# Kernel tuning notes

Measured on AMD Instinct MI355X. Metric: run time of the kernel, lower is better.

The kernel has to match this reference:

```python
import jax, jax.numpy as jnp
import numpy as np

N, E, B, P = 131072, 262144, 4096, 1024
HID, CTX, FEAT, L = 256, 128, 512, 4


def _ln(x, g, bb, eps=1e-5):
    mu = jnp.mean(x, -1, keepdims=True)
    v = jnp.mean((x - mu) ** 2, -1, keepdims=True)
    return (x - mu) * jax.lax.rsqrt(v + eps) * g + bb


def setup_inputs() -> dict:
    key = jax.random.key(0)
    ks = iter(jax.random.split(key, 64))
    nrm = lambda sh, s=0.05: (jax.random.normal(next(ks), sh, jnp.float32) * s)
    inp = {
        "nf": jax.random.normal(next(ks), (N, 69), jnp.float32),
        "ei": jax.random.randint(next(ks), (2, E), 0, N, dtype=jnp.int32),
        "ef": jax.random.normal(next(ks), (E, 9), jnp.float32),
        "b": jnp.sort(jax.random.randint(next(ks), (N,), 0, B, dtype=jnp.int32)),
        "pid": jax.random.randint(next(ks), (B,), 0, P, dtype=jnp.int32),
        # MPNN params
        "Wn": nrm((69, HID)), "bn": jnp.zeros((HID,)),
        "We": nrm((9, HID)), "be": jnp.zeros((HID,)),
        "Wm": nrm((L, 2 * HID, HID)), "bm": jnp.zeros((L, HID)),
        "Wu": nrm((L, HID, HID)), "bu": jnp.zeros((L, HID)),
        "lng": jnp.ones((L, HID)), "lnb": jnp.zeros((L, HID)),
        # context embedding
        "ctx_emb": nrm((P, CTX), 0.02),
        # FiLM gamma net: Linear(128,256)-LN-ReLU-Linear(256,512)
        "gW1": nrm((CTX, HID)), "gb1": jnp.zeros((HID,)),
        "glng": jnp.ones((HID,)), "glnb": jnp.zeros((HID,)),
        "gW2": nrm((HID, FEAT)), "gb2": jnp.ones((FEAT,)),
        # FiLM beta net
        "bW1": nrm((CTX, HID)), "bb1": jnp.zeros((HID,)),
        "blng": jnp.ones((HID,)), "blnb": jnp.zeros((HID,)),
        "bW2": nrm((HID, FEAT)), "bb2": jnp.zeros((FEAT,)),
        # predictor: Linear(512,256)-ReLU-Linear(256,1)
        "pW1": nrm((FEAT, HID)), "pb1": jnp.zeros((HID,)),
        "pW2": nrm((HID, 1)), "pb2": jnp.zeros((1,)),
    }
    return inp


def reference(nf, ei, ef, b, pid, Wn, bn, We, be, Wm, bm, Wu, bu, lng, lnb,
              ctx_emb, gW1, gb1, glng, glnb, gW2, gb2,
              bW1, bb1, blng, blnb, bW2, bb2, pW1, pb1, pW2, pb2):
    src, dst = ei[0], ei[1]
    h = jax.nn.relu(nf @ Wn + bn)          # [N,256]
    e = jax.nn.relu(ef @ We + be)          # [E,256]
    for l in range(L):
        m = jax.nn.relu(jnp.concatenate([h[src], e], -1) @ Wm[l] + bm[l])  # [E,256]
        agg = jax.ops.segment_sum(m, dst, num_segments=N)                   # scatter-add
        h = _ln(h + jax.nn.relu(agg @ Wu[l] + bu[l]), lng[l], lnb[l])
    # graph readout: mean || max -> [B,512]
    ssum = jax.ops.segment_sum(h, b, num_segments=B)
    cnt = jnp.maximum(jax.ops.segment_sum(jnp.ones((h.shape[0], 1), h.dtype), b, num_segments=B), 1.0)
    gmax = jax.ops.segment_max(h, b, num_segments=B)
    gmax = jnp.where(jnp.isneginf(gmax), 0.0, gmax)
    g = jnp.concatenate([ssum / cnt, gmax], -1)  # [B,512]
    # FiLM fusion
    c = ctx_emb[pid]                              # [B,128]
    gamma = jax.nn.relu(_ln(c @ gW1 + gb1, glng, glnb)) @ gW2 + gb2
    beta = jax.nn.relu(_ln(c @ bW1 + bb1, blng, blnb)) @ bW2 + bb2
    hmod = gamma * g + beta
    out = (jax.nn.relu(hmod @ pW1 + pb1) @ pW2 + pb2).squeeze(-1)  # [B]
    return out
```

## Files before the change

kernel.cpp:

```cpp
#include <hip/hip_runtime.h>
#include <hip/hip_bf16.h>
#include <math.h>

#define HID 256
#define CTXD 128
#define FEAT 512
#define NLAYER 4

#define SW(n) (((n) >> 1) & 3)

typedef __hip_bfloat16 bf16;
typedef __attribute__((ext_vector_type(8))) short short8;
typedef __attribute__((ext_vector_type(4))) float floatx4;

__device__ __forceinline__ float bf2f(bf16 x) { return __bfloat162float(x); }
__device__ __forceinline__ bf16 f2bf(float x) { return __float2bfloat16(x); }
__device__ __forceinline__ float us2f(unsigned short u) {
    union { unsigned u; float f; } c; c.u = ((unsigned)u) << 16; return c.f;
}
__device__ __forceinline__ unsigned short f2us(float f) {
    bf16 b = f2bf(f); return *(unsigned short*)&b;
}

__device__ __forceinline__ void glds16(const void* g, void* l) {
    __builtin_amdgcn_global_load_lds(
        (__attribute__((address_space(1))) void*)g,
        (__attribute__((address_space(3))) void*)l, 16, 0, 0);
}

__global__ __launch_bounds__(256) void hist_kernel(const int* __restrict__ dst,
                                                   int* __restrict__ cnt, int E)
{
    int i = blockIdx.x * 256 + threadIdx.x;
    if (i < E) atomicAdd(&cnt[dst[i]], 1);
}

__global__ __launch_bounds__(256) void scan1_kernel(int* __restrict__ cnt,
                                                    int* __restrict__ bsum)
{
    __shared__ int sd[256];
    const int t = threadIdx.x;
    const int i = blockIdx.x * 256 + t;
    int v = cnt[i];
    sd[t] = v;
    __syncthreads();
    for (int o = 1; o < 256; o <<= 1) {
        int x = (t >= o) ? sd[t - o] : 0;
        __syncthreads();
        sd[t] += x;
        __syncthreads();
    }
    cnt[i] = sd[t] - v;
    if (t == 255) bsum[blockIdx.x] = sd[255];
}

__global__ void scan2_kernel(int* __restrict__ bsum)
{
    __shared__ int sd[512];
    const int t = threadIdx.x;
    int v = bsum[t];
    sd[t] = v;
    __syncthreads();
    for (int o = 1; o < 512; o <<= 1) {
        int x = (t >= o) ? sd[t - o] : 0;
        __syncthreads();
        sd[t] += x;
        __syncthreads();
    }
    bsum[t] = sd[t] - v;
}

__global__ __launch_bounds__(256) void scan3_kernel(int* __restrict__ cnt,
                                                    const int* __restrict__ bsum)
{
    int i = blockIdx.x * 256 + threadIdx.x;
    cnt[i] += bsum[blockIdx.x];
}

__global__ __launch_bounds__(256) void scatter_perm_kernel(
    const int* __restrict__ dst, int* __restrict__ cursor,
    int* __restrict__ perm, int E)
{
    int i = blockIdx.x * 256 + threadIdx.x;
    if (i < E) {
        int p = atomicAdd(&cursor[dst[i]], 1);
        perm[p] = i;
    }
}

__global__ __launch_bounds__(256)
void build_wimg_kernel(const float* __restrict__ W, bf16* __restrict__ img,
                       int K, int KT, int L)
{
    long idx = (long)blockIdx.x * 256 + threadIdx.x;
    long tot = (long)L * KT * 8192;
    if (idx >= tot) return;
    int l  = (int)(idx / ((long)KT * 8192));
    int r  = (int)(idx % ((long)KT * 8192));
    int kt = r >> 13;
    int r2 = r & 8191;
    int n  = r2 >> 5;
    int s  = (r2 >> 3) & 3;
    int j  = r2 & 7;
    int k  = kt * 32 + ((s ^ SW(n)) * 8) + j;
    float v = (k < K) ? W[((long)l * K + k) * HID + n] : 0.f;
    img[idx] = f2bf(v);
}

__global__ __launch_bounds__(512)
void msg_gemm3(const bf16* __restrict__ h_, const float* __restrict__ ef,
               const float* __restrict__ We, const float* __restrict__ be,
               const int* __restrict__ src, const int* __restrict__ perm,
               const float* __restrict__ W, const bf16* __restrict__ Wimg,
               const float* __restrict__ bias, bf16* __restrict__ mout)
{
    __shared__ __align__(16) short As[128 * 32];
    __shared__ __align__(16) short Bs[256 * 32];
    __shared__ int   srcL[128];
    __shared__ int   edgeL[128];
    __shared__ float efL[128][9];

    const int  t  = threadIdx.x;
    const long bm = (long)blockIdx.x * 128;

    if (t < 128) {
        int eg = perm[bm + t];
        edgeL[t] = eg;
        srcL[t]  = src[eg];
    }
    __syncthreads();
    for (int i = t; i < 128 * 9; i += 512) {
        int r = i / 9, qq = i % 9;
        efL[r][qq] = ef[(long)edgeL[r] * 9 + qq];
    }
    __syncthreads();

    floatx4 acc[4][4];
#pragma unroll
    for (int i = 0; i < 4; ++i)
#pragma unroll
        for (int j = 0; j < 4; ++j) acc[i][j] = (floatx4){0.f, 0.f, 0.f, 0.f};

    const int w = t >> 6, lane = t & 63;
    const int fr = lane & 15, q = lane >> 4;
    const int wm = (w & 1) * 64, wn = (w >> 1) * 64;
    const int arow = t >> 2, akg = t & 3;

    for (int kt = 0; kt < 16; ++kt) {
        const int k0 = kt * 32;
        {
            const int kk = k0 + akg * 8;
            short8 pk;
            if (kk < HID) {
                pk = *(const short8*)((const short*)h_ +
                                      ((long)srcL[arow] * HID + kk));
            } else {
                const int kc = kk - HID;
                float s[8];
#pragma unroll
                for (int j = 0; j < 8; ++j) s[j] = be[kc + j];
#pragma unroll
                for (int qq = 0; qq < 9; ++qq) {
                    const float efv = efL[arow][qq];
#pragma unroll
                    for (int j = 0; j < 8; ++j)
                        s[j] = fmaf(efv, We[qq * HID + kc + j], s[j]);
                }
#pragma unroll
                for (int j = 0; j < 8; ++j) pk[j] = (short)f2us(fmaxf(s[j], 0.f));
            }
            *(short8*)&As[arow * 32 + (akg ^ SW(arow)) * 8] = pk;
        }
        if (Wimg) {
            const short* base = (const short*)Wimg + (long)kt * 8192;
#pragma unroll
            for (int j = 0; j < 2; ++j) {
                const int chunk = w * 2 + j;
                glds16(base + chunk * 512 + lane * 8, (char*)Bs + chunk * 1024);
            }
        } else {
#pragma unroll
            for (int cc = 0; cc < 2; ++cc) {
                const int slot = t + cc * 512;
                const int n    = slot >> 2;
                const int kg   = slot & 3;
                const int kk   = k0 + kg * 8;
                short8 pk;
#pragma unroll
                for (int j = 0; j < 8; ++j)
                    pk[j] = (short)f2us(W[(long)(kk + j) * HID + n]);
                *(short8*)&Bs[n * 32 + (kg ^ SW(n)) * 8] = pk;
            }
        }
        __syncthreads();
        short8 af[4], bf8[4];
#pragma unroll
        for (int mt = 0; mt < 4; ++mt) {
            const int r = wm + mt * 16 + fr;
            af[mt] = *(const short8*)&As[r * 32 + (q ^ SW(r)) * 8];
        }
#pragma unroll
        for (int nt = 0; nt < 4; ++nt) {
            const int r = wn + nt * 16 + fr;
            bf8[nt] = *(const short8*)&Bs[r * 32 + (q ^ SW(r)) * 8];
        }
#pragma unroll
        for (int mt = 0; mt < 4; ++mt)
#pragma unroll
            for (int nt = 0; nt < 4; ++nt)
                acc[mt][nt] = __builtin_amdgcn_mfma_f32_16x16x32_bf16(
                    af[mt], bf8[nt], acc[mt][nt], 0, 0, 0);
        __syncthreads();
    }

#pragma unroll
    for (int nt = 0; nt < 4; ++nt) {
        const int col = wn + nt * 16 + fr;
        const float bv = bias[col];
#pragma unroll
        for (int mt = 0; mt < 4; ++mt)
#pragma unroll
            for (int reg = 0; reg < 4; ++reg) {
                const long row = bm + wm + mt * 16 + q * 4 + reg;
                mout[row * HID + col] = f2bf(fmaxf(acc[mt][nt][reg] + bv, 0.f));
            }
    }
}

__global__ __launch_bounds__(512)
void upd_gemm3(const bf16* __restrict__ mbuf, const int* __restrict__ cursor,
               const float* __restrict__ W, const bf16* __restrict__ Wimg,
               const float* __restrict__ bias,
               const float* __restrict__ lng, const float* __restrict__ lnb,
               bf16* __restrict__ h_)
{
    __shared__ __align__(16) short As[128 * 32];
    __shared__ __align__(16) short Bs[256 * 32];
    __shared__ int   rpL[129];
    __shared__ float redS[128][4];
    __shared__ float redS2[128][4];

    const int  t  = threadIdx.x;
    const long bm = (long)blockIdx.x * 128;

    if (t < 128) rpL[t + 1] = cursor[bm + t];
    if (t == 0)  rpL[0] = (bm == 0) ? 0 : cursor[bm - 1];
    __syncthreads();

    floatx4 acc[4][4];
#pragma unroll
    for (int i = 0; i < 4; ++i)
#pragma unroll
        for (int j = 0; j < 4; ++j) acc[i][j] = (floatx4){0.f, 0.f, 0.f, 0.f};

    const int w = t >> 6, lane = t & 63;
    const int fr = lane & 15, q = lane >> 4;
    const int wm = (w & 1) * 64, wn = (w >> 1) * 64;
    const int arow = t >> 2, akg = t & 3;

    for (int kt = 0; kt < 8; ++kt) {
        const int k0 = kt * 32;
        {
            const int kk = k0 + akg * 8;
            float s[8] = {0.f, 0.f, 0.f, 0.f, 0.f, 0.f, 0.f, 0.f};
            const int j1 = rpL[arow + 1];
            for (int j = rpL[arow]; j < j1; ++j) {
                const short8 mv = *(const short8*)((const short*)mbuf +
                                                   ((long)j * HID + kk));
#pragma unroll
                for (int x = 0; x < 8; ++x) s[x] += us2f((unsigned short)mv[x]);
            }
            short8 pk;
#pragma unroll
            for (int x = 0; x < 8; ++x) pk[x] = (short)f2us(s[x]);
            *(short8*)&As[arow * 32 + (akg ^ SW(arow)) * 8] = pk;
        }
        if (Wimg) {
            const short* base = (const short*)Wimg + (long)kt * 8192;
#pragma unroll
            for (int j = 0; j < 2; ++j) {
                const int chunk = w * 2 + j;
                glds16(base + chunk * 512 + lane * 8, (char*)Bs + chunk * 1024);
            }
        } else {
#pragma unroll
            for (int cc = 0; cc < 2; ++cc) {
                const int slot = t + cc * 512;
                const int n    = slot >> 2;
                const int kg   = slot & 3;
                const int kk   = k0 + kg * 8;
                short8 pk;
#pragma unroll
                for (int j = 0; j < 8; ++j)
                    pk[j] = (short)f2us(W[(long)(kk + j) * HID + n]);
                *(short8*)&Bs[n * 32 + (kg ^ SW(n)) * 8] = pk;
            }
        }
        __syncthreads();
        short8 af[4], bf8[4];
#pragma unroll
        for (int mt = 0; mt < 4; ++mt) {
            const int r = wm + mt * 16 + fr;
            af[mt] = *(const short8*)&As[r * 32 + (q ^ SW(r)) * 8];
        }
#pragma unroll
        for (int nt = 0; nt < 4; ++nt) {
            const int r = wn + nt * 16 + fr;
            bf8[nt] = *(const short8*)&Bs[r * 32 + (q ^ SW(r)) * 8];
        }
#pragma unroll
        for (int mt = 0; mt < 4; ++mt)
#pragma unroll
            for (int nt = 0; nt < 4; ++nt)
                acc[mt][nt] = __builtin_amdgcn_mfma_f32_16x16x32_bf16(
                    af[mt], bf8[nt], acc[mt][nt], 0, 0, 0);
        __syncthreads();
    }

    const int wnIdx = w >> 1;
#pragma unroll
    for (int mt = 0; mt < 4; ++mt)
#pragma unroll
        for (int reg = 0; reg < 4; ++reg) {
            const int  lrow = wm + mt * 16 + q * 4 + reg;
            const long row  = bm + lrow;
            float ps = 0.f, ps2 = 0.f;
#pragma unroll
            for (int nt = 0; nt < 4; ++nt) {
                const int col = wn + nt * 16 + fr;
                float v = bf2f(h_[row * HID + col]) +
                          fmaxf(acc[mt][nt][reg] + bias[col], 0.f);
                acc[mt][nt][reg] = v;
                ps  += v;
                ps2 += v * v;
            }
#pragma unroll
            for (int m = 1; m < 16; m <<= 1) {
                ps  += __shfl_xor(ps, m);
                ps2 += __shfl_xor(ps2, m);
            }
            if (fr == 0) { redS[lrow][wnIdx] = ps; redS2[lrow][wnIdx] = ps2; }
        }
    __syncthreads();
#pragma unroll
    for (int mt = 0; mt < 4; ++mt)
#pragma unroll
        for (int reg = 0; reg < 4; ++reg) {
            const int  lrow = wm + mt * 16 + q * 4 + reg;
            const long row  = bm + lrow;
            const float ts  = redS[lrow][0] + redS[lrow][1] +
                              redS[lrow][2] + redS[lrow][3];
            const float ts2 = redS2[lrow][0] + redS2[lrow][1] +
                              redS2[lrow][2] + redS2[lrow][3];
            const float mu  = ts * (1.f / 256.f);
            const float var = ts2 * (1.f / 256.f) - mu * mu;
            const float rs  = rsqrtf(var + 1e-5f);
#pragma unroll
            for (int nt = 0; nt < 4; ++nt) {
                const int col = wn + nt * 16 + fr;
                const float y = (acc[mt][nt][reg] - mu) * rs * lng[col] + lnb[col];
                h_[row * HID + col] = f2bf(y);
            }
        }
}

__global__ __launch_bounds__(512)
void enc_gemm3(const float* __restrict__ nf, const bf16* __restrict__ Wimg,
               const float* __restrict__ bias, bf16* __restrict__ h_)
{
    __shared__ __align__(16) short As[128 * 32];
    __shared__ __align__(16) short Bs[256 * 32];

    const int  t  = threadIdx.x;
    const long bm = (long)blockIdx.x * 128;

    floatx4 acc[4][4];
#pragma unroll
    for (int i = 0; i < 4; ++i)
#pragma unroll
        for (int j = 0; j < 4; ++j) acc[i][j] = (floatx4){0.f, 0.f, 0.f, 0.f};

    const int w = t >> 6, lane = t & 63;
    const int fr = lane & 15, q = lane >> 4;
    const int wm = (w & 1) * 64, wn = (w >> 1) * 64;
    const int arow = t >> 2, akg = t & 3;

    for (int kt = 0; kt < 3; ++kt) {
        const int k0 = kt * 32;
        {
            const int kk = k0 + akg * 8;
            short8 pk;
#pragma unroll
            for (int j = 0; j < 8; ++j) {
                const int k = kk + j;
                pk[j] = (short)f2us((k < 69) ? nf[(bm + arow) * 69 + k] : 0.f);
            }
            *(short8*)&As[arow * 32 + (akg ^ SW(arow)) * 8] = pk;
        }
        const short* base = (const short*)Wimg + (long)kt * 8192;
#pragma unroll
        for (int j = 0; j < 2; ++j) {
            const int chunk = w * 2 + j;
            glds16(base + chunk * 512 + lane * 8, (char*)Bs + chunk * 1024);
        }
        __syncthreads();
        short8 af[4], bf8[4];
#pragma unroll
        for (int mt = 0; mt < 4; ++mt) {
            const int r = wm + mt * 16 + fr;
            af[mt] = *(const short8*)&As[r * 32 + (q ^ SW(r)) * 8];
        }
#pragma unroll
        for (int nt = 0; nt < 4; ++nt) {
            const int r = wn + nt * 16 + fr;
            bf8[nt] = *(const short8*)&Bs[r * 32 + (q ^ SW(r)) * 8];
        }
#pragma unroll
        for (int mt = 0; mt < 4; ++mt)
#pragma unroll
            for (int nt = 0; nt < 4; ++nt)
                acc[mt][nt] = __builtin_amdgcn_mfma_f32_16x16x32_bf16(
                    af[mt], bf8[nt], acc[mt][nt], 0, 0, 0);
        __syncthreads();
    }

#pragma unroll
    for (int nt = 0; nt < 4; ++nt) {
        const int col = wn + nt * 16 + fr;
        const float bv = bias[col];
#pragma unroll
        for (int mt = 0; mt < 4; ++mt)
#pragma unroll
            for (int reg = 0; reg < 4; ++reg) {
                const long row = bm + wm + mt * 16 + q * 4 + reg;
                h_[row * HID + col] = f2bf(fmaxf(acc[mt][nt][reg] + bv, 0.f));
            }
    }
}

struct PlainF32 {
    const float* A; int lda;
    __device__ float operator()(int r, int k) const { return A[(long)r * lda + k]; }
};
struct CtxF32 {
    const float* ctx; const int* pid;
    __device__ float operator()(int r, int k) const {
        return ctx[(long)pid[r] * CTXD + k];
    }
};
struct StoreF32 {
    float* C; int ldc; int relu;
    __device__ void operator()(int r, int c, const float* v) const {
        float4 o;
        o.x = v[0]; o.y = v[1]; o.z = v[2]; o.w = v[3];
        if (relu) {
            o.x = fmaxf(o.x, 0.f); o.y = fmaxf(o.y, 0.f);
            o.z = fmaxf(o.z, 0.f); o.w = fmaxf(o.w, 0.f);
        }
        *(float4*)&C[(long)r * ldc + c] = o;
    }
};
struct StoreBf16Relu {
    bf16* C;
    __device__ void operator()(int r, int c, const float* v) const {
        bf16 tmp[4];
#pragma unroll
        for (int j = 0; j < 4; ++j) tmp[j] = f2bf(fmaxf(v[j], 0.f));
        *(ushort4*)&C[(long)r * HID + c] = *(const ushort4*)tmp;
    }
};

template <typename Loader, typename Epi>
__global__ __launch_bounds__(256)
void gemm_tiled(Loader loader, const float* __restrict__ W,
                const float* __restrict__ bias, Epi epi, int M, int K, int Nc)
{
    constexpr int BM = 64, BN = 64, BK = 16;
    __shared__ __align__(16) float As[BK][BM + 4];
    __shared__ __align__(16) float Ws[BK][BN];

    const int bm = blockIdx.x * BM;
    const int bn = blockIdx.y * BN;
    const int t  = threadIdx.x;
    const int arow = t >> 2, akq = (t & 3) * 4;
    const int wn = t & 63, wk0 = t >> 6;
    const int tx = t & 15, ty = t >> 4;

    float acc[4][4] = {};
    const int ntiles = (K + BK - 1) / BK;
    for (int kt = 0; kt < ntiles; ++kt) {
        const int k0 = kt * BK;
#pragma unroll
        for (int i = 0; i < 4; ++i) {
            int k = k0 + akq + i;
            As[akq + i][arow] = (k < K) ? loader(bm + arow, k) : 0.f;
        }
#pragma unroll
        for (int i = 0; i < 4; ++i) {
            int kr = wk0 + i * 4;
            int k  = k0 + kr;
            Ws[kr][wn] = (k < K) ? W[(long)k * Nc + bn + wn] : 0.f;
        }
        __syncthreads();
#pragma unroll
        for (int kk = 0; kk < BK; ++kk) {
            float4 a = *(const float4*)&As[kk][ty * 4];
            float4 b = *(const float4*)&Ws[kk][tx * 4];
            float av[4] = {a.x, a.y, a.z, a.w};
            float bv[4] = {b.x, b.y, b.z, b.w};
#pragma unroll
            for (int i = 0; i < 4; ++i)
#pragma unroll
                for (int j = 0; j < 4; ++j) acc[i][j] += av[i] * bv[j];
        }
        __syncthreads();
    }
#pragma unroll
    for (int i = 0; i < 4; ++i) {
        const int row = bm + ty * 4 + i;
        const int col = bn + tx * 4;
        float v[4];
#pragma unroll
        for (int j = 0; j < 4; ++j) v[j] = acc[i][j] + bias[col + j];
        epi(row, col, v);
    }
}

__global__ __launch_bounds__(256)
void ln_f32_relu_kernel(float* __restrict__ x, const float* __restrict__ g,
                        const float* __restrict__ bb)
{
    const long row = blockIdx.x;
    const int  j   = threadIdx.x;
    float v = x[row * HID + j];
    float s = v, s2 = v * v;
#pragma unroll
    for (int o = 32; o > 0; o >>= 1) {
        s  += __shfl_down(s, o);
        s2 += __shfl_down(s2, o);
    }
    __shared__ float red[2][4];
    const int wid = j >> 6, lane = j & 63;
    if (lane == 0) { red[0][wid] = s; red[1][wid] = s2; }
    __syncthreads();
    float ts  = red[0][0] + red[0][1] + red[0][2] + red[0][3];
    float ts2 = red[1][0] + red[1][1] + red[1][2] + red[1][3];
    float mu  = ts * (1.f / 256.f);
    float var = ts2 * (1.f / 256.f) - mu * mu;
    float y = (v - mu) * rsqrtf(var + 1e-5f) * g[j] + bb[j];
    x[row * HID + j] = fmaxf(y, 0.f);
}

__device__ int lower_bound_i(const int* __restrict__ arr, int n, int val)
{
    int lo = 0, hi = n;
    while (lo < hi) {
        int mid = (lo + hi) >> 1;
        if (arr[mid] < val) lo = mid + 1; else hi = mid;
    }
    return lo;
}

__global__ __launch_bounds__(256)
void readout_kernel(const bf16* __restrict__ h, const int* __restrict__ b,
                    float* __restrict__ gout, int Nn)
{
    const int gidx = blockIdx.x;
    const int j    = threadIdx.x;
    const int lo   = lower_bound_i(b, Nn, gidx);
    const int hi   = lower_bound_i(b, Nn, gidx + 1);
    float s = 0.f, mx = -INFINITY;
    for (int n = lo; n < hi; ++n) {
        float v = bf2f(h[(long)n * HID + j]);
        s += v;
        mx = fmaxf(mx, v);
    }
    const int cnt = hi - lo;
    gout[(long)gidx * FEAT + j]       = s / fmaxf((float)cnt, 1.f);
    gout[(long)gidx * FEAT + HID + j] = (cnt > 0) ? mx : 0.f;
}

__global__ __launch_bounds__(256)
void film_mod_kernel(const float* __restrict__ gamma, float* __restrict__ g,
                     const float* __restrict__ beta, int n)
{
    int i = blockIdx.x * 256 + threadIdx.x;
    if (i < n) g[i] = gamma[i] * g[i] + beta[i];
}

__global__ __launch_bounds__(256)
void final_dot_kernel(const float* __restrict__ ph, const float* __restrict__ w,
                      const float* __restrict__ b2, float* __restrict__ out)
{
    const int row  = blockIdx.x * 4 + (threadIdx.x >> 6);
    const int lane = threadIdx.x & 63;
    float s = 0.f;
#pragma unroll
    for (int k = lane; k < HID; k += 64)
        s += ph[(long)row * HID + k] * w[k];
#pragma unroll
    for (int o = 32; o > 0; o >>= 1) s += __shfl_down(s, o);
    if (lane == 0) out[row] = s + b2[0];
}

__global__ void diag_out_kernel(float* out, int n, float wsmb)
{
    int i = blockIdx.x * 256 + threadIdx.x;
    if (i < n) out[i] = (i == 0) ? wsmb : 0.f;
}

extern "C" void kernel_launch(void* const* d_in, const int* in_sizes, int n_in,
                              void* d_out, int out_size, void* d_ws, size_t ws_size,
                              hipStream_t stream)
{
    const int N = 131072, E = 262144, B = 4096;

    const float* nf   = (const float*)d_in[0];
    const int*   ei   = (const int*)  d_in[1];
    const float* ef   = (const float*)d_in[2];
    const int*   bidx = (const int*)  d_in[3];
    const int*   pid  = (const int*)  d_in[4];
    const float* Wn   = (const float*)d_in[5];
    const float* bn   = (const float*)d_in[6];
    const float* We   = (const float*)d_in[7];
    const float* be   = (const float*)d_in[8];
    const float* Wm   = (const float*)d_in[9];
    const float* bm   = (const float*)d_in[10];
    const float* Wu   = (const float*)d_in[11];
    const float* bu   = (const float*)d_in[12];
    const float* lng  = (const float*)d_in[13];
    const float* lnb  = (const float*)d_in[14];
    const float* ctx  = (const float*)d_in[15];
    const float* gW1  = (const float*)d_in[16];
    const float* gb1  = (const float*)d_in[17];
    const float* glng = (const float*)d_in[18];
    const float* glnb = (const float*)d_in[19];
    const float* gW2  = (const float*)d_in[20];
    const float* gb2  = (const float*)d_in[21];
    const float* bW1  = (const float*)d_in[22];
    const float* bb1  = (const float*)d_in[23];
    const float* blng = (const float*)d_in[24];
    const float* blnb = (const float*)d_in[25];
    const float* bW2  = (const float*)d_in[26];
    const float* bb2  = (const float*)d_in[27];
    const float* pW1  = (const float*)d_in[28];
    const float* pb1  = (const float*)d_in[29];
    const float* pW2  = (const float*)d_in[30];
    const float* pb2  = (const float*)d_in[31];

    const int* src = ei;
    const int* dst = ei + E;
    float* out = (float*)d_out;

    const size_t hB    = (size_t)N * HID * sizeof(bf16);
    const size_t mB    = (size_t)E * HID * sizeof(bf16);
    const size_t curB  = (size_t)N * 4;
    const size_t permB = (size_t)E * 4;
    const size_t bsumB = 2048 * 4;
    const size_t wmImgB = (size_t)NLAYER * 16 * 8192 * 2;
    const size_t wuImgB = (size_t)NLAYER * 8  * 8192 * 2;
    const size_t wnImgB = (size_t)3 * 8192 * 2;

    const size_t needBase = hB + mB + curB + permB + bsumB;
    const size_t needFull = needBase + wmImgB + wuImgB + wnImgB;

    if (ws_size < needBase) {
        diag_out_kernel<<<dim3((B + 255) / 256), dim3(256), 0, stream>>>(
            out, B, (float)(ws_size >> 20));
        return;
    }
    const bool haveImg = ws_size >= needFull;

    char* p = (char*)d_ws;
    bf16* h      = (bf16*)p;  p += hB;
    bf16* mbuf   = (bf16*)p;  p += mB;
    int*  cursor = (int*)p;   p += curB;
    int*  perm   = (int*)p;   p += permB;
    int*  bsum   = (int*)p;   p += bsumB;
    bf16* wmImg = nullptr; bf16* wuImg = nullptr; bf16* wnImg = nullptr;
    if (haveImg) {
        wmImg = (bf16*)p; p += wmImgB;
        wuImg = (bf16*)p; p += wuImgB;
        wnImg = (bf16*)p; p += wnImgB;
    }

    float* gbuf  = (float*)mbuf;
    float* t1    = gbuf  + (long)B * FEAT;
    float* t2    = t1    + (long)B * HID;
    float* gamma = t2    + (long)B * HID;
    float* beta  = gamma + (long)B * FEAT;
    float* ph    = beta  + (long)B * FEAT;

    dim3 blk(256), blk5(512);

    hipMemsetAsync(cursor, 0, curB, stream);
    hist_kernel<<<dim3(E / 256), blk, 0, stream>>>(dst, cursor, E);
    scan1_kernel<<<dim3(N / 256), blk, 0, stream>>>(cursor, bsum);
    scan2_kernel<<<dim3(1), dim3(512), 0, stream>>>(bsum);
    scan3_kernel<<<dim3(N / 256), blk, 0, stream>>>(cursor, bsum);
    scatter_perm_kernel<<<dim3(E / 256), blk, 0, stream>>>(dst, cursor, perm, E);

    if (haveImg) {
        build_wimg_kernel<<<dim3((NLAYER * 16 * 8192 + 255) / 256), blk, 0, stream>>>(
            Wm, wmImg, 2 * HID, 16, NLAYER);
        build_wimg_kernel<<<dim3((NLAYER * 8 * 8192 + 255) / 256), blk, 0, stream>>>(
            Wu, wuImg, HID, 8, NLAYER);
        build_wimg_kernel<<<dim3((3 * 8192 + 255) / 256), blk, 0, stream>>>(
            Wn, wnImg, 69, 3, 1);
    }

    if (haveImg) {
        enc_gemm3<<<dim3(N / 128), blk5, 0, stream>>>(nf, wnImg, bn, h);
    } else {
        gemm_tiled<<<dim3(N / 64, HID / 64), blk, 0, stream>>>(
            PlainF32{nf, 69}, Wn, bn, StoreBf16Relu{h}, N, 69, HID);
    }

    for (int l = 0; l < NLAYER; ++l) {
        const float* Wml  = Wm  + (long)l * 2 * HID * HID;
        const float* bml  = bm  + (long)l * HID;
        const float* Wul  = Wu  + (long)l * HID * HID;
        const float* bul  = bu  + (long)l * HID;
        const float* lngl = lng + (long)l * HID;
        const float* lnbl = lnb + (long)l * HID;
        const bf16* wmI = haveImg ? wmImg + (long)l * 16 * 8192 : nullptr;
        const bf16* wuI = haveImg ? wuImg + (long)l * 8 * 8192 : nullptr;

        msg_gemm3<<<dim3(E / 128), blk5, 0, stream>>>(
            h, ef, We, be, src, perm, Wml, wmI, bml, mbuf);
        upd_gemm3<<<dim3(N / 128), blk5, 0, stream>>>(
            mbuf, cursor, Wul, wuI, bul, lngl, lnbl, h);
    }

    readout_kernel<<<dim3(B), blk, 0, stream>>>(h, bidx, gbuf, N);

    gemm_tiled<<<dim3(B / 64, HID / 64), blk, 0, stream>>>(
        CtxF32{ctx, pid}, gW1, gb1, StoreF32{t1, HID, 0}, B, CTXD, HID);
    ln_f32_relu_kernel<<<dim3(B), blk, 0, stream>>>(t1, glng, glnb);
    gemm_tiled<<<dim3(B / 64, FEAT / 64), blk, 0, stream>>>(
        PlainF32{t1, HID}, gW2, gb2, StoreF32{gamma, FEAT, 0}, B, HID, FEAT);

    gemm_tiled<<<dim3(B / 64, HID / 64), blk, 0, stream>>>(
        CtxF32{ctx, pid}, bW1, bb1, StoreF32{t2, HID, 0}, B, CTXD, HID);
    ln_f32_relu_kernel<<<dim3(B), blk, 0, stream>>>(t2, blng, blnb);
    gemm_tiled<<<dim3(B / 64, FEAT / 64), blk, 0, stream>>>(
        PlainF32{t2, HID}, bW2, bb2, StoreF32{beta, FEAT, 0}, B, HID, FEAT);

    film_mod_kernel<<<dim3((B * FEAT + 255) / 256), blk, 0, stream>>>(
        gamma, gbuf, beta, B * FEAT);
    gemm_tiled<<<dim3(B / 64, HID / 64), blk, 0, stream>>>(
        PlainF32{gbuf, FEAT}, pW1, pb1, StoreF32{ph, HID, 1}, B, FEAT, HID);
    final_dot_kernel<<<dim3(B / 4), blk, 0, stream>>>(ph, pW2, pb2, out);
}
```

Before: 2.004 ms.

## Precompute node-side message GEMM and fuse edge messages with segmented aggregation

The message GEMM is split algebraically. The h[src] half of Wm is applied once per node (N rows) rather than once per edge (E rows), and the result is gathered per edge and combined with the edge-feature half. A new msg_agg kernel walks the dst-sorted edges of 64 destination nodes, computes the edge-half GEMM plus bias and ReLU in shared memory, and sums the messages per node directly. This removes the E×256 message buffer round trip and the separate gather-sum in the update kernel. In exchange, the node projection is rounded to bf16 before the sum, and blocks with many edges loop over chunks, which can cause load imbalance.

```diff
diff --git a/kernel.cpp b/kernel.cpp
--- a/kernel.cpp
+++ b/kernel.cpp
@@ -107,33 +107,119 @@
     img[idx] = f2bf(v);
 }
 
+__device__ __forceinline__ void kt_tail512(
+    int kt, const bf16* __restrict__ Wimg, const float* __restrict__ W,
+    short* As, short* Bs, floatx4 (&acc)[4][4])
+{
+    const int t = threadIdx.x;
+    const int w = t >> 6, lane = t & 63;
+    const int fr = lane & 15, q = lane >> 4;
+    const int wm = (w & 1) * 64, wn = (w >> 1) * 64;
+    const int k0 = kt * 32;
+
+    if (Wimg) {
+        const short* base = (const short*)Wimg + (long)kt * 8192;
+#pragma unroll
+        for (int j = 0; j < 2; ++j) {
+            const int chunk = w * 2 + j;
+            glds16(base + chunk * 512 + lane * 8, (char*)Bs + chunk * 1024);
+        }
+    } else {
+#pragma unroll
+        for (int cc = 0; cc < 2; ++cc) {
+            const int slot = t + cc * 512;
+            const int n    = slot >> 2;
+            const int kg   = slot & 3;
+            const int kk   = k0 + kg * 8;
+            short8 pk;
+#pragma unroll
+            for (int j = 0; j < 8; ++j)
+                pk[j] = (short)f2us(W[(long)(kk + j) * HID + n]);
+            *(short8*)&Bs[n * 32 + (kg ^ SW(n)) * 8] = pk;
+        }
+    }
+    __syncthreads();
+    short8 af[4], bf8[4];
+#pragma unroll
+    for (int mt = 0; mt < 4; ++mt) {
+        const int r = wm + mt * 16 + fr;
+        af[mt] = *(const short8*)&As[r * 32 + (q ^ SW(r)) * 8];
+    }
+#pragma unroll
+    for (int nt = 0; nt < 4; ++nt) {
+        const int r = wn + nt * 16 + fr;
+        bf8[nt] = *(const short8*)&Bs[r * 32 + (q ^ SW(r)) * 8];
+    }
+#pragma unroll
+    for (int mt = 0; mt < 4; ++mt)
+#pragma unroll
+        for (int nt = 0; nt < 4; ++nt)
+            acc[mt][nt] = __builtin_amdgcn_mfma_f32_16x16x32_bf16(
+                af[mt], bf8[nt], acc[mt][nt], 0, 0, 0);
+    __syncthreads();
+}
+
+__device__ __forceinline__ void kt_tail256(
+    int kt, const bf16* __restrict__ Wimg, const float* __restrict__ W,
+    short* As, short* Bs, floatx4 (&acc)[4][4])
+{
+    const int t = threadIdx.x;
+    const int w = t >> 6, lane = t & 63;
+    const int fr = lane & 15, q = lane >> 4;
+    const int wn = w * 64;
+    const int k0 = kt * 32;
+
+    if (Wimg) {
+        const short* base = (const short*)Wimg + (long)kt * 8192;
+#pragma unroll
+        for (int j = 0; j < 4; ++j) {
+            const int chunk = w * 4 + j;
+            glds16(base + chunk * 512 + lane * 8, (char*)Bs + chunk * 1024);
+        }
+    } else {
+#pragma unroll
+        for (int cc = 0; cc < 4; ++cc) {
+            const int slot = t + cc * 256;
+            const int n    = slot >> 2;
+            const int kg   = slot & 3;
+            const int kk   = k0 + kg * 8;
+            short8 pk;
+#pragma unroll
+            for (int j = 0; j < 8; ++j)
+                pk[j] = (short)f2us(W[(long)(kk + j) * HID + n]);
+            *(short8*)&Bs[n * 32 + (kg ^ SW(n)) * 8] = pk;
+        }
+    }
+    __syncthreads();
+    short8 af[4], bf8[4];
+#pragma unroll
+    for (int mt = 0; mt < 4; ++mt) {
+        const int r = mt * 16 + fr;
+        af[mt] = *(const short8*)&As[r * 32 + (q ^ SW(r)) * 8];
+    }
+#pragma unroll
+    for (int nt = 0; nt < 4; ++nt) {
+        const int r = wn + nt * 16 + fr;
+        bf8[nt] = *(const short8*)&Bs[r * 32 + (q ^ SW(r)) * 8];
+    }
+#pragma unroll
+    for (int mt = 0; mt < 4; ++mt)
+#pragma unroll
+        for (int nt = 0; nt < 4; ++nt)
+            acc[mt][nt] = __builtin_amdgcn_mfma_f32_16x16x32_bf16(
+                af[mt], bf8[nt], acc[mt][nt], 0, 0, 0);
+    __syncthreads();
+}
+
 __global__ __launch_bounds__(512)
-void msg_gemm3(const bf16* __restrict__ h_, const float* __restrict__ ef,
-               const float* __restrict__ We, const float* __restrict__ be,
-               const int* __restrict__ src, const int* __restrict__ perm,
-               const float* __restrict__ W, const bf16* __restrict__ Wimg,
-               const float* __restrict__ bias, bf16* __restrict__ mout)
+void ht_gemm(const bf16* __restrict__ h_, const float* __restrict__ W,
+             const bf16* __restrict__ Wimg, bf16* __restrict__ ht)
 {
     __shared__ __align__(16) short As[128 * 32];
     __shared__ __align__(16) short Bs[256 * 32];
-    __shared__ int   srcL[128];
-    __shared__ int   edgeL[128];
-    __shared__ float efL[128][9];
 
     const int  t  = threadIdx.x;
     const long bm = (long)blockIdx.x * 128;
-
-    if (t < 128) {
-        int eg = perm[bm + t];
-        edgeL[t] = eg;
-        srcL[t]  = src[eg];
-    }
-    __syncthreads();
-    for (int i = t; i < 128 * 9; i += 512) {
-        int r = i / 9, qq = i % 9;
-        efL[r][qq] = ef[(long)edgeL[r] * 9 + qq];
-    }
-    __syncthreads();
 
     floatx4 acc[4][4];
 #pragma unroll
@@ -145,90 +231,157 @@
     const int fr = lane & 15, q = lane >> 4;
     const int wm = (w & 1) * 64, wn = (w >> 1) * 64;
     const int arow = t >> 2, akg = t & 3;
-
-    for (int kt = 0; kt < 16; ++kt) {
-        const int k0 = kt * 32;
-        {
-            const int kk = k0 + akg * 8;
-            short8 pk;
-            if (kk < HID) {
-                pk = *(const short8*)((const short*)h_ +
-                                      ((long)srcL[arow] * HID + kk));
-            } else {
-                const int kc = kk - HID;
-                float s[8];
-#pragma unroll
-                for (int j = 0; j < 8; ++j) s[j] = be[kc + j];
-#pragma unroll
-                for (int qq = 0; qq < 9; ++qq) {
-                    const float efv = efL[arow][qq];
-#pragma unroll
-                    for (int j = 0; j < 8; ++j)
-                        s[j] = fmaf(efv, We[qq * HID + kc + j], s[j]);
-                }
-#pragma unroll
-                for (int j = 0; j < 8; ++j) pk[j] = (short)f2us(fmaxf(s[j], 0.f));
-            }
-            *(short8*)&As[arow * 32 + (akg ^ SW(arow)) * 8] = pk;
-        }
-        if (Wimg) {
-            const short* base = (const short*)Wimg + (long)kt * 8192;
-#pragma unroll
-            for (int j = 0; j < 2; ++j) {
-                const int chunk = w * 2 + j;
-                glds16(base + chunk * 512 + lane * 8, (char*)Bs + chunk * 1024);
-            }
-        } else {
-#pragma unroll
-            for (int cc = 0; cc < 2; ++cc) {
-                const int slot = t + cc * 512;
-                const int n    = slot >> 2;
-                const int kg   = slot & 3;
-                const int kk   = k0 + kg * 8;
-                short8 pk;
-#pragma unroll
-                for (int j = 0; j < 8; ++j)
-                    pk[j] = (short)f2us(W[(long)(kk + j) * HID + n]);
-                *(short8*)&Bs[n * 32 + (kg ^ SW(n)) * 8] = pk;
-            }
-        }
-        __syncthreads();
-        short8 af[4], bf8[4];
-#pragma unroll
-        for (int mt = 0; mt < 4; ++mt) {
-            const int r = wm + mt * 16 + fr;
-            af[mt] = *(const short8*)&As[r * 32 + (q ^ SW(r)) * 8];
-        }
-#pragma unroll
-        for (int nt = 0; nt < 4; ++nt) {
-            const int r = wn + nt * 16 + fr;
-            bf8[nt] = *(const short8*)&Bs[r * 32 + (q ^ SW(r)) * 8];
-        }
-#pragma unroll
-        for (int mt = 0; mt < 4; ++mt)
-#pragma unroll
-            for (int nt = 0; nt < 4; ++nt)
-                acc[mt][nt] = __builtin_amdgcn_mfma_f32_16x16x32_bf16(
-                    af[mt], bf8[nt], acc[mt][nt], 0, 0, 0);
-        __syncthreads();
+    const int aslot = arow * 32 + (akg ^ SW(arow)) * 8;
+
+    for (int kt = 0; kt < 8; ++kt) {
+        const int kk = kt * 32 + akg * 8;
+        short8 v = *(const short8*)((const short*)h_ + (bm + arow) * HID + kk);
+        *(short8*)&As[aslot] = v;
+        kt_tail512(kt, Wimg, W, As, Bs, acc);
     }
 
 #pragma unroll
     for (int nt = 0; nt < 4; ++nt) {
         const int col = wn + nt * 16 + fr;
-        const float bv = bias[col];
 #pragma unroll
         for (int mt = 0; mt < 4; ++mt)
 #pragma unroll
             for (int reg = 0; reg < 4; ++reg) {
                 const long row = bm + wm + mt * 16 + q * 4 + reg;
-                mout[row * HID + col] = f2bf(fmaxf(acc[mt][nt][reg] + bv, 0.f));
+                ht[row * HID + col] = f2bf(acc[mt][nt][reg]);
             }
     }
 }
 
+__global__ __launch_bounds__(256)
+void msg_agg(const bf16* __restrict__ ht, const float* __restrict__ ef,
+             const float* __restrict__ We, const float* __restrict__ be,
+             const int* __restrict__ src, const int* __restrict__ perm,
+             const int* __restrict__ cursor,
+             const float* __restrict__ W, const bf16* __restrict__ Wimg,
+             const float* __restrict__ bias, bf16* __restrict__ agg)
+{
+    __shared__ __align__(16) short As[64 * 32];
+    __shared__ __align__(16) short Bs[256 * 32];
+    __shared__ __align__(16) short htL[64 * 256];
+    __shared__ int   rpL[65];
+    __shared__ int   srcL[64];
+    __shared__ int   edgeL[64];
+    __shared__ float efL[64][9];
+
+    const int t  = threadIdx.x;
+    const int n0 = blockIdx.x * 64;
+
+    if (t < 64) rpL[t + 1] = cursor[n0 + t];
+    if (t == 0) rpL[0] = (n0 == 0) ? 0 : cursor[n0 - 1];
+    __syncthreads();
+    const int j0 = rpL[0], j1 = rpL[64];
+    int nch = (j1 - j0 + 63) >> 6;
+    if (nch < 1) nch = 1;
+
+    const int w = t >> 6, lane = t & 63;
+    const int fr = lane & 15, q = lane >> 4;
+    const int wn = w * 64;
+    const int arow = t >> 2, akg = t & 3;
+    const int aslot = arow * 32 + (akg ^ SW(arow)) * 8;
+    const int srow = t >> 2, ssg = t & 3;
+
+    for (int ch = 0; ch < nch; ++ch) {
+        const int jc = j0 + ch * 64;
+        if (t < 64) {
+            const int j = jc + t;
+            const int eg = (j < j1) ? perm[j] : 0;
+            edgeL[t] = eg;
+            srcL[t]  = src[eg];
+        }
+        __syncthreads();
+        for (int i = t; i < 64 * 9; i += 256) {
+            const int r = i / 9, qq = i % 9;
+            efL[r][qq] = (jc + r < j1) ? ef[(long)edgeL[r] * 9 + qq] : 0.f;
+        }
+        short8 stash[8];
+        {
+            const short* hp = (const short*)ht + (long)srcL[srow] * HID + ssg * 64;
+#pragma unroll
+            for (int i = 0; i < 8; ++i) stash[i] = *(const short8*)(hp + i * 8);
+        }
+        __syncthreads();
+
+        floatx4 acc[4][4];
+#pragma unroll
+        for (int i = 0; i < 4; ++i)
+#pragma unroll
+            for (int j = 0; j < 4; ++j) acc[i][j] = (floatx4){0.f, 0.f, 0.f, 0.f};
+
+        for (int kt = 0; kt < 8; ++kt) {
+            const int kc = kt * 32 + akg * 8;
+            float sv[8];
+#pragma unroll
+            for (int j = 0; j < 8; ++j) sv[j] = be[kc + j];
+#pragma unroll
+            for (int qq = 0; qq < 9; ++qq) {
+                const float efv = efL[arow][qq];
+#pragma unroll
+                for (int j = 0; j < 8; ++j)
+                    sv[j] = fmaf(efv, We[qq * HID + kc + j], sv[j]);
+            }
+            short8 pk;
+#pragma unroll
+            for (int j = 0; j < 8; ++j) pk[j] = (short)f2us(fmaxf(sv[j], 0.f));
+            *(short8*)&As[aslot] = pk;
+            kt_tail256(kt, Wimg, W, As, Bs, acc);
+        }
+
+        {
+            short* hl = &htL[srow * 256 + ssg * 64];
+#pragma unroll
+            for (int i = 0; i < 8; ++i) *(short8*)(hl + i * 8) = stash[i];
+        }
+        __syncthreads();
+
+#pragma unroll
+        for (int nt = 0; nt < 4; ++nt) {
+            const int col = wn + nt * 16 + fr;
+            const float bv = bias[col];
+#pragma unroll
+            for (int mt = 0; mt < 4; ++mt)
+#pragma unroll
+                for (int reg = 0; reg < 4; ++reg) {
+                    const int rl = mt * 16 + q * 4 + reg;
+                    const float v = fmaxf(acc[mt][nt][reg] + bv +
+                                          us2f((unsigned short)htL[rl * 256 + col]), 0.f);
+                    htL[rl * 256 + col] = (short)f2us(v);
+                }
+        }
+        __syncthreads();
+
+        for (int nn = 0; nn < 16; ++nn) {
+            const int nl = w * 16 + nn;
+            int a = rpL[nl]     - jc; if (a < 0)  a = 0;
+            int b = rpL[nl + 1] - jc; if (b > 64) b = 64;
+            float s0 = 0.f, s1 = 0.f, s2 = 0.f, s3 = 0.f;
+            for (int r = a; r < b; ++r) {
+                const ushort4 hv = *(const ushort4*)&htL[r * 256 + lane * 4];
+                s0 += us2f(hv.x); s1 += us2f(hv.y);
+                s2 += us2f(hv.z); s3 += us2f(hv.w);
+            }
+            bf16* ap = agg + (long)(n0 + nl) * HID + lane * 4;
+            if (ch == 0) {
+                unsigned short o[4] = {f2us(s0), f2us(s1), f2us(s2), f2us(s3)};
+                *(ushort4*)ap = *(const ushort4*)o;
+            } else if (b > a) {
+                const ushort4 ov = *(const ushort4*)ap;
+                unsigned short o[4] = {f2us(s0 + us2f(ov.x)), f2us(s1 + us2f(ov.y)),
+                                       f2us(s2 + us2f(ov.z)), f2us(s3 + us2f(ov.w))};
+                *(ushort4*)ap = *(const ushort4*)o;
+            }
+        }
+        __syncthreads();
+    }
+}
+
 __global__ __launch_bounds__(512)
-void upd_gemm3(const bf16* __restrict__ mbuf, const int* __restrict__ cursor,
+void upd_gemm5(const bf16* __restrict__ agg,
                const float* __restrict__ W, const bf16* __restrict__ Wimg,
                const float* __restrict__ bias,
                const float* __restrict__ lng, const float* __restrict__ lnb,
@@ -236,16 +389,11 @@
 {
     __shared__ __align__(16) short As[128 * 32];
     __shared__ __align__(16) short Bs[256 * 32];
-    __shared__ int   rpL[129];
     __shared__ float redS[128][4];
     __shared__ float redS2[128][4];
 
     const int  t  = threadIdx.x;
     const long bm = (long)blockIdx.x * 128;
-
-    if (t < 128) rpL[t + 1] = cursor[bm + t];
-    if (t == 0)  rpL[0] = (bm == 0) ? 0 : cursor[bm - 1];
-    __syncthreads();
 
     floatx4 acc[4][4];
 #pragma unroll
@@ -257,64 +405,13 @@
     const int fr = lane & 15, q = lane >> 4;
     const int wm = (w & 1) * 64, wn = (w >> 1) * 64;
     const int arow = t >> 2, akg = t & 3;
+    const int aslot = arow * 32 + (akg ^ SW(arow)) * 8;
 
     for (int kt = 0; kt < 8; ++kt) {
-        const int k0 = kt * 32;
-        {
-            const int kk = k0 + akg * 8;
-            float s[8] = {0.f, 0.f, 0.f, 0.f, 0.f, 0.f, 0.f, 0.f};
-            const int j1 = rpL[arow + 1];
-            for (int j = rpL[arow]; j < j1; ++j) {
-                const short8 mv = *(const short8*)((const short*)mbuf +
-                                                   ((long)j * HID + kk));
-#pragma unroll
-                for (int x = 0; x < 8; ++x) s[x] += us2f((unsigned short)mv[x]);
-            }
-            short8 pk;
-#pragma unroll
-            for (int x = 0; x < 8; ++x) pk[x] = (short)f2us(s[x]);
-            *(short8*)&As[arow * 32 + (akg ^ SW(arow)) * 8] = pk;
-        }
-        if (Wimg) {
-            const short* base = (const short*)Wimg + (long)kt * 8192;
-#pragma unroll
-            for (int j = 0; j < 2; ++j) {
-                const int chunk = w * 2 + j;
-                glds16(base + chunk * 512 + lane * 8, (char*)Bs + chunk * 1024);
-            }
-        } else {
-#pragma unroll
-            for (int cc = 0; cc < 2; ++cc) {
-                const int slot = t + cc * 512;
-                const int n    = slot >> 2;
-                const int kg   = slot & 3;
-                const int kk   = k0 + kg * 8;
-                short8 pk;
-#pragma unroll
-                for (int j = 0; j < 8; ++j)
-                    pk[j] = (short)f2us(W[(long)(kk + j) * HID + n]);
-                *(short8*)&Bs[n * 32 + (kg ^ SW(n)) * 8] = pk;
-            }
-        }
-        __syncthreads();
-        short8 af[4], bf8[4];
-#pragma unroll
-        for (int mt = 0; mt < 4; ++mt) {
-            const int r = wm + mt * 16 + fr;
-            af[mt] = *(const short8*)&As[r * 32 + (q ^ SW(r)) * 8];
-        }
-#pragma unroll
-        for (int nt = 0; nt < 4; ++nt) {
-            const int r = wn + nt * 16 + fr;
-            bf8[nt] = *(const short8*)&Bs[r * 32 + (q ^ SW(r)) * 8];
-        }
-#pragma unroll
-        for (int mt = 0; mt < 4; ++mt)
-#pragma unroll
-            for (int nt = 0; nt < 4; ++nt)
-                acc[mt][nt] = __builtin_amdgcn_mfma_f32_16x16x32_bf16(
-                    af[mt], bf8[nt], acc[mt][nt], 0, 0, 0);
-        __syncthreads();
+        const int kk = kt * 32 + akg * 8;
+        short8 v = *(const short8*)((const short*)agg + (bm + arow) * HID + kk);
+        *(short8*)&As[aslot] = v;
+        kt_tail512(kt, Wimg, W, As, Bs, acc);
     }
 
     const int wnIdx = w >> 1;
@@ -384,44 +481,18 @@
     const int fr = lane & 15, q = lane >> 4;
     const int wm = (w & 1) * 64, wn = (w >> 1) * 64;
     const int arow = t >> 2, akg = t & 3;
+    const int aslot = arow * 32 + (akg ^ SW(arow)) * 8;
 
     for (int kt = 0; kt < 3; ++kt) {
-        const int k0 = kt * 32;
-        {
-            const int kk = k0 + akg * 8;
-            short8 pk;
-#pragma unroll
-            for (int j = 0; j < 8; ++j) {
-                const int k = kk + j;
-                pk[j] = (short)f2us((k < 69) ? nf[(bm + arow) * 69 + k] : 0.f);
-            }
-            *(short8*)&As[arow * 32 + (akg ^ SW(arow)) * 8] = pk;
-        }
-        const short* base = (const short*)Wimg + (long)kt * 8192;
-#pragma unroll
-        for (int j = 0; j < 2; ++j) {
-            const int chunk = w * 2 + j;
-            glds16(base + chunk * 512 + lane * 8, (char*)Bs + chunk * 1024);
-        }
-        __syncthreads();
-        short8 af[4], bf8[4];
-#pragma unroll
-        for (int mt = 0; mt < 4; ++mt) {
-            const int r = wm + mt * 16 + fr;
-            af[mt] = *(const short8*)&As[r * 32 + (q ^ SW(r)) * 8];
-        }
-#pragma unroll
-        for (int nt = 0; nt < 4; ++nt) {
-            const int r = wn + nt * 16 + fr;
-            bf8[nt] = *(const short8*)&Bs[r * 32 + (q ^ SW(r)) * 8];
-        }
-#pragma unroll
-        for (int mt = 0; mt < 4; ++mt)
-#pragma unroll
-            for (int nt = 0; nt < 4; ++nt)
-                acc[mt][nt] = __builtin_amdgcn_mfma_f32_16x16x32_bf16(
-                    af[mt], bf8[nt], acc[mt][nt], 0, 0, 0);
-        __syncthreads();
+        const int kk = kt * 32 + akg * 8;
+        short8 pk;
+#pragma unroll
+        for (int j = 0; j < 8; ++j) {
+            const int k = kk + j;
+            pk[j] = (short)f2us((k < 69) ? nf[(bm + arow) * 69 + k] : 0.f);
+        }
+        *(short8*)&As[aslot] = pk;
+        kt_tail512(kt, Wimg, nullptr, As, Bs, acc);
     }
 
 #pragma unroll
@@ -653,7 +724,8 @@
     float* out = (float*)d_out;
 
     const size_t hB    = (size_t)N * HID * sizeof(bf16);
-    const size_t mB    = (size_t)E * HID * sizeof(bf16);
+    const size_t htB   = (size_t)N * HID * sizeof(bf16);
+    const size_t aggB  = (size_t)N * HID * sizeof(bf16);
     const size_t curB  = (size_t)N * 4;
     const size_t permB = (size_t)E * 4;
     const size_t bsumB = 2048 * 4;
@@ -661,7 +733,7 @@
     const size_t wuImgB = (size_t)NLAYER * 8  * 8192 * 2;
     const size_t wnImgB = (size_t)3 * 8192 * 2;
 
-    const size_t needBase = hB + mB + curB + permB + bsumB;
+    const size_t needBase = hB + htB + aggB + curB + permB + bsumB;
     const size_t needFull = needBase + wmImgB + wuImgB + wnImgB;
 
     if (ws_size < needBase) {
@@ -673,7 +745,8 @@
 
     char* p = (char*)d_ws;
     bf16* h      = (bf16*)p;  p += hB;
-    bf16* mbuf   = (bf16*)p;  p += mB;
+    bf16* ht     = (bf16*)p;  p += htB;
+    bf16* agg    = (bf16*)p;  p += aggB;
     int*  cursor = (int*)p;   p += curB;
     int*  perm   = (int*)p;   p += permB;
     int*  bsum   = (int*)p;   p += bsumB;
@@ -684,7 +757,7 @@
         wnImg = (bf16*)p; p += wnImgB;
     }
 
-    float* gbuf  = (float*)mbuf;
+    float* gbuf  = (float*)ht;
     float* t1    = gbuf  + (long)B * FEAT;
     float* t2    = t1    + (long)B * HID;
     float* gamma = t2    + (long)B * HID;
@@ -718,18 +791,21 @@
 
     for (int l = 0; l < NLAYER; ++l) {
         const float* Wml  = Wm  + (long)l * 2 * HID * HID;
+        const float* WmlB = Wml + (long)HID * HID;
         const float* bml  = bm  + (long)l * HID;
         const float* Wul  = Wu  + (long)l * HID * HID;
         const float* bul  = bu  + (long)l * HID;
         const float* lngl = lng + (long)l * HID;
         const float* lnbl = lnb + (long)l * HID;
-        const bf16* wmI = haveImg ? wmImg + (long)l * 16 * 8192 : nullptr;
-        const bf16* wuI = haveImg ? wuImg + (long)l * 8 * 8192 : nullptr;
-
-        msg_gemm3<<<dim3(E / 128), blk5, 0, stream>>>(
-            h, ef, We, be, src, perm, Wml, wmI, bml, mbuf);
-        upd_gemm3<<<dim3(N / 128), blk5, 0, stream>>>(
-            mbuf, cursor, Wul, wuI, bul, lngl, lnbl, h);
+        const bf16* wmTopI = haveImg ? wmImg + (long)l * 16 * 8192 : nullptr;
+        const bf16* wmBotI = haveImg ? wmImg + (long)l * 16 * 8192 + 8 * 8192 : nullptr;
+        const bf16* wuI    = haveImg ? wuImg + (long)l * 8 * 8192 : nullptr;
+
+        ht_gemm<<<dim3(N / 128), blk5, 0, stream>>>(h, Wml, wmTopI, ht);
+        msg_agg<<<dim3(N / 64), blk, 0, stream>>>(
+            ht, ef, We, be, src, perm, cursor, WmlB, wmBotI, bml, agg);
+        upd_gemm5<<<dim3(N / 128), blk5, 0, stream>>>(
+            agg, Wul, wuI, bul, lngl, lnbl, h);
     }
 
     readout_kernel<<<dim3(B), blk, 0, stream>>>(h, bidx, gbuf, N);
```

After: 2.146 ms. 7.1% more time.
